# Kernel tuning notes

Hardware: AMD Instinct MI355X
Metric: run time of the kernel (lower is better)

## Reference

```python
import jax, jax.numpy as jnp
import numpy as np

NEG_SLOPE = 0.01  # F.leaky_relu default
EPS = 1e-12       # F.normalize default eps

def _lrelu(h):
    return jnp.where(h > 0, h, NEG_SLOPE * h)

def setup_inputs() -> dict:
    key = jax.random.key(0)
    ks = jax.random.split(key, 16)
    N, E, D = 100000, 800000, 64
    x = jax.random.normal(ks[0], (N, D), dtype=jnp.float32)
    src = jax.random.randint(ks[1], (E,), 0, N, dtype=jnp.int32)
    dst = jax.random.randint(ks[2], (E,), 0, N, dtype=jnp.int32)
    def lin(k, fo, fi):
        k1, k2 = jax.random.split(k)
        s = 1.0 / np.sqrt(fi)
        w = jax.random.uniform(k1, (fo, fi), jnp.float32, -s, s)
        b = jax.random.uniform(k2, (fo,), jnp.float32, -s, s)
        return w, b
    w1, b1 = lin(ks[3], 256, D)
    w2, b2 = lin(ks[4], 128, 256)
    w3, b3 = lin(ks[5], 64, 128)
    w4, b4 = lin(ks[6], 1, 64)
    w_self, _ = lin(ks[7], D, D)   # SAGEConv fc_self (no bias)
    w_neigh, _ = lin(ks[8], D, D)  # SAGEConv fc_neigh (no bias)
    bias = jnp.zeros((D,), jnp.float32)  # SAGEConv bias param
    return dict(x=x, src=src, dst=dst, w1=w1, b1=b1, w2=w2, b2=b2,
                w3=w3, b3=b3, w4=w4, b4=b4,
                w_self=w_self, w_neigh=w_neigh, bias=bias)

def reference(x, src, dst, w1, b1, w2, b2, w3, b3, w4, b4, w_self, w_neigh, bias):
    N = x.shape[0]
    # per-edge score MLP on (h_u - h_v)
    d = x[src] - x[dst]                       # [E, D]
    h = _lrelu(d @ w1.T + b1)                 # [E, 256]
    h = _lrelu(h @ w2.T + b2)                 # [E, 128]
    h = _lrelu(h @ w3.T + b3)                 # [E, 64]
    e = jax.nn.sigmoid(h @ w4.T + b4)         # [E, 1]
    # SAGEConv 'mean' with edge weights: mean over incoming edges of e * x_src
    msg = e * x[src]                          # [E, D]
    s = jax.ops.segment_sum(msg, dst, num_segments=N)               # [N, D]
    deg = jax.ops.segment_sum(jnp.ones((src.shape[0],), x.dtype), dst,
                              num_segments=N)                        # [N]
    neigh = s / jnp.maximum(deg, 1.0)[:, None]
    A = x @ w_self.T + neigh @ w_neigh.T + bias
    A = _lrelu(A)
    norm = jnp.maximum(jnp.linalg.norm(A, axis=1, keepdims=True), EPS)
    A = A / norm
    return A, e
```

## Files before the change

kernel.cpp:

```cpp
#include <hip/hip_runtime.h>
#include <hip/hip_bf16.h>

typedef unsigned short u16;
typedef unsigned int   u32;
typedef __attribute__((ext_vector_type(8))) short short8;
typedef __attribute__((ext_vector_type(4))) float f32x4;

__device__ __forceinline__ u16 f2bf(float f) {
  u32 u = __float_as_uint(f);
  u += 0x7FFFu + ((u >> 16) & 1u);
  return (u16)(u >> 16);
}
__device__ __forceinline__ float bf2f(u16 h) { return __uint_as_float(((u32)h) << 16); }
__device__ __forceinline__ u32 pk2(float lo, float hi) {
  union { __hip_bfloat162 h; u32 u; } c;
  c.h = __float22bfloat162_rn(make_float2(lo, hi));
  return c.u;
}
__device__ __forceinline__ float lo16f(u32 u) { return __uint_as_float(u << 16); }
__device__ __forceinline__ float hi16f(u32 u) { return __uint_as_float(u & 0xffff0000u); }
__device__ __forceinline__ float lrelu(float v) { return v > 0.f ? v : 0.01f * v; }

__host__ __device__ __forceinline__ int sig(int c) {
  return ((c >> 5) << 5) | ((c & 12) << 1) | (((c >> 4) & 1) << 2) | (c & 3);
}

union U8 { u32 w[4]; short8 v; };

#define MFMA16(A, B, C) __builtin_amdgcn_mfma_f32_16x16x32_bf16(A, B, C, 0, 0, 0)

#define W2_BASE 2048
#define W3_BASE 6144
#define NCHUNK8 7168


__global__ __launch_bounds__(512, 2) void edge_mlp(
    const float* __restrict__ x, const int* __restrict__ src, const int* __restrict__ dst,
    const short8* __restrict__ wcat,
    const float* __restrict__ b1p, const float* __restrict__ b2p, const float* __restrict__ b3p,
    const float* __restrict__ w4p, const float* __restrict__ b4,
    const int* __restrict__ rowptr, const int* __restrict__ ord,
    u16* __restrict__ msgbuf, float* __restrict__ eout, int E)
{
  __shared__ short8 ldsw[NCHUNK8];
  const int tid  = threadIdx.x;
  const int lane = tid & 63;
  const int wv   = tid >> 6;
  const int g    = lane >> 4;
  const int r    = lane & 15;
  const int eb   = (blockIdx.x * 8 + wv) * 32;
  const int e0   = eb + r, e1 = eb + 16 + r;
  const int ec0  = e0 < E ? e0 : E - 1;
  const int ec1  = e1 < E ? e1 : E - 1;
  const int sn0 = src[ec0], dn0 = dst[ec0];
  const int sn1 = src[ec1], dn1 = dst[ec1];
  const float b4v = b4[0];

  const float* xsr0 = x + (size_t)sn0 * 64 + 8 * g;
  const float* xdr0 = x + (size_t)dn0 * 64 + 8 * g;
  const float* xsr1 = x + (size_t)sn1 * 64 + 8 * g;
  const float* xdr1 = x + (size_t)dn1 * 64 + 8 * g;
  const float4 a0s0 = *(const float4*)(xsr0),      a0s1 = *(const float4*)(xsr0 + 4);
  const float4 a0s2 = *(const float4*)(xsr0 + 32), a0s3 = *(const float4*)(xsr0 + 36);
  const float4 a0d0 = *(const float4*)(xdr0),      a0d1 = *(const float4*)(xdr0 + 4);
  const float4 a0d2 = *(const float4*)(xdr0 + 32), a0d3 = *(const float4*)(xdr0 + 36);
  const float4 a1s0 = *(const float4*)(xsr1),      a1s1 = *(const float4*)(xsr1 + 4);
  const float4 a1s2 = *(const float4*)(xsr1 + 32), a1s3 = *(const float4*)(xsr1 + 36);
  const float4 a1d0 = *(const float4*)(xdr1),      a1d1 = *(const float4*)(xdr1 + 4);
  const float4 a1d2 = *(const float4*)(xdr1 + 32), a1d3 = *(const float4*)(xdr1 + 36);
  const int pos0 = rowptr[dn0] + ord[ec0];
  const int pos1 = rowptr[dn1] + ord[ec1];

  {
    const short8* gp = wcat + wv * 64 + lane;
    short8*       lp = ldsw + wv * 64;
#pragma unroll
    for (int i = 0; i < 14; i++) {
      __builtin_amdgcn_global_load_lds(
          (const __attribute__((address_space(1))) u32*)(gp + i * 512),
          (__attribute__((address_space(3))) u32*)(lp + i * 512), 16, 0, 0);
    }
  }
  __syncthreads();

  U8 bA0, bB0, bA1, bB1, sA0lo, sA0hi, sA1lo, sA1hi;
  bA0.w[0] = pk2(a0s0.x - a0d0.x, a0s0.y - a0d0.y);
  bA0.w[1] = pk2(a0s0.z - a0d0.z, a0s0.w - a0d0.w);
  bA0.w[2] = pk2(a0s1.x - a0d1.x, a0s1.y - a0d1.y);
  bA0.w[3] = pk2(a0s1.z - a0d1.z, a0s1.w - a0d1.w);
  bB0.w[0] = pk2(a0s2.x - a0d2.x, a0s2.y - a0d2.y);
  bB0.w[1] = pk2(a0s2.z - a0d2.z, a0s2.w - a0d2.w);
  bB0.w[2] = pk2(a0s3.x - a0d3.x, a0s3.y - a0d3.y);
  bB0.w[3] = pk2(a0s3.z - a0d3.z, a0s3.w - a0d3.w);
  bA1.w[0] = pk2(a1s0.x - a1d0.x, a1s0.y - a1d0.y);
  bA1.w[1] = pk2(a1s0.z - a1d0.z, a1s0.w - a1d0.w);
  bA1.w[2] = pk2(a1s1.x - a1d1.x, a1s1.y - a1d1.y);
  bA1.w[3] = pk2(a1s1.z - a1d1.z, a1s1.w - a1d1.w);
  bB1.w[0] = pk2(a1s2.x - a1d2.x, a1s2.y - a1d2.y);
  bB1.w[1] = pk2(a1s2.z - a1d2.z, a1s2.w - a1d2.w);
  bB1.w[2] = pk2(a1s3.x - a1d3.x, a1s3.y - a1d3.y);
  bB1.w[3] = pk2(a1s3.z - a1d3.z, a1s3.w - a1d3.w);
  sA0lo.w[0] = pk2(a0s0.x, a0s0.y); sA0lo.w[1] = pk2(a0s0.z, a0s0.w);
  sA0lo.w[2] = pk2(a0s1.x, a0s1.y); sA0lo.w[3] = pk2(a0s1.z, a0s1.w);
  sA0hi.w[0] = pk2(a0s2.x, a0s2.y); sA0hi.w[1] = pk2(a0s2.z, a0s2.w);
  sA0hi.w[2] = pk2(a0s3.x, a0s3.y); sA0hi.w[3] = pk2(a0s3.z, a0s3.w);
  sA1lo.w[0] = pk2(a1s0.x, a1s0.y); sA1lo.w[1] = pk2(a1s0.z, a1s0.w);
  sA1lo.w[2] = pk2(a1s1.x, a1s1.y); sA1lo.w[3] = pk2(a1s1.z, a1s1.w);
  sA1hi.w[0] = pk2(a1s2.x, a1s2.y); sA1hi.w[1] = pk2(a1s2.z, a1s2.w);
  sA1hi.w[2] = pk2(a1s3.x, a1s3.y); sA1hi.w[3] = pk2(a1s3.z, a1s3.w);

  U8 h1A[8], h1B[8];
  {
    const float* b1l = b1p + 4 * g;
#pragma unroll
    for (int t = 0; t < 16; t++) {
      short8 a0 = ldsw[(t * 2 + 0) * 64 + lane];
      short8 a1 = ldsw[(t * 2 + 1) * 64 + lane];
      f32x4 p = {}, q = {};
      p = MFMA16(a0, bA0.v, p); p = MFMA16(a1, bB0.v, p);
      q = MFMA16(a0, bA1.v, q); q = MFMA16(a1, bB1.v, q);
      float4 bb = *(const float4*)(b1l + 16 * t);
      const int w0 = 2 * t, w1 = 2 * t + 1;
      h1A[w0 >> 2].w[w0 & 3] = pk2(lrelu(p[0] + bb.x), lrelu(p[1] + bb.y));
      h1A[w1 >> 2].w[w1 & 3] = pk2(lrelu(p[2] + bb.z), lrelu(p[3] + bb.w));
      h1B[w0 >> 2].w[w0 & 3] = pk2(lrelu(q[0] + bb.x), lrelu(q[1] + bb.y));
      h1B[w1 >> 2].w[w1 & 3] = pk2(lrelu(q[2] + bb.z), lrelu(q[3] + bb.w));
    }
  }

  U8 h2A[4], h2B[4];
  {
    const float* b2l = b2p + 4 * g;
#pragma unroll
    for (int t = 0; t < 8; t++) {
      f32x4 p = {}, q = {};
#pragma unroll
      for (int s = 0; s < 8; s++) {
        short8 a = ldsw[W2_BASE + (t * 8 + s) * 64 + lane];
        p = MFMA16(a, h1A[s].v, p);
        q = MFMA16(a, h1B[s].v, q);
      }
      float4 bb = *(const float4*)(b2l + 16 * t);
      const int w0 = 2 * t, w1 = 2 * t + 1;
      h2A[w0 >> 2].w[w0 & 3] = pk2(lrelu(p[0] + bb.x), lrelu(p[1] + bb.y));
      h2A[w1 >> 2].w[w1 & 3] = pk2(lrelu(p[2] + bb.z), lrelu(p[3] + bb.w));
      h2B[w0 >> 2].w[w0 & 3] = pk2(lrelu(q[0] + bb.x), lrelu(q[1] + bb.y));
      h2B[w1 >> 2].w[w1 & 3] = pk2(lrelu(q[2] + bb.z), lrelu(q[3] + bb.w));
    }
  }

  float dot0 = 0.f, dot1 = 0.f;
  {
    const float* b3l = b3p + 4 * g;
    const float* w4l = w4p + 4 * g;
#pragma unroll
    for (int t = 0; t < 4; t++) {
      f32x4 p = {}, q = {};
#pragma unroll
      for (int s = 0; s < 4; s++) {
        short8 a = ldsw[W3_BASE + (t * 4 + s) * 64 + lane];
        p = MFMA16(a, h2A[s].v, p);
        q = MFMA16(a, h2B[s].v, q);
      }
      float4 bb = *(const float4*)(b3l + 16 * t);
      float4 ww = *(const float4*)(w4l + 16 * t);
      dot0 += lrelu(p[0] + bb.x) * ww.x + lrelu(p[1] + bb.y) * ww.y
            + lrelu(p[2] + bb.z) * ww.z + lrelu(p[3] + bb.w) * ww.w;
      dot1 += lrelu(q[0] + bb.x) * ww.x + lrelu(q[1] + bb.y) * ww.y
            + lrelu(q[2] + bb.z) * ww.z + lrelu(q[3] + bb.w) * ww.w;
    }
  }
  dot0 += __shfl_xor(dot0, 16); dot0 += __shfl_xor(dot0, 32);
  dot1 += __shfl_xor(dot1, 16); dot1 += __shfl_xor(dot1, 32);
  const float ev0 = 1.f / (1.f + __expf(-(dot0 + b4v)));
  const float ev1 = 1.f / (1.f + __expf(-(dot1 + b4v)));

  if (g == 0) {
    if (e0 < E) eout[e0] = ev0;
    if (e1 < E) eout[e1] = ev1;
  }
  if (e0 < E) {
    u16* mp = msgbuf + (size_t)pos0 * 64 + g * 16;
    U8 m;
    m.w[0] = pk2(ev0 * lo16f(sA0lo.w[0]), ev0 * hi16f(sA0lo.w[0]));
    m.w[1] = pk2(ev0 * lo16f(sA0lo.w[1]), ev0 * hi16f(sA0lo.w[1]));
    m.w[2] = pk2(ev0 * lo16f(sA0lo.w[2]), ev0 * hi16f(sA0lo.w[2]));
    m.w[3] = pk2(ev0 * lo16f(sA0lo.w[3]), ev0 * hi16f(sA0lo.w[3]));
    *(short8*)(mp) = m.v;
    m.w[0] = pk2(ev0 * lo16f(sA0hi.w[0]), ev0 * hi16f(sA0hi.w[0]));
    m.w[1] = pk2(ev0 * lo16f(sA0hi.w[1]), ev0 * hi16f(sA0hi.w[1]));
    m.w[2] = pk2(ev0 * lo16f(sA0hi.w[2]), ev0 * hi16f(sA0hi.w[2]));
    m.w[3] = pk2(ev0 * lo16f(sA0hi.w[3]), ev0 * hi16f(sA0hi.w[3]));
    *(short8*)(mp + 8) = m.v;
  }
  if (e1 < E) {
    u16* mp = msgbuf + (size_t)pos1 * 64 + g * 16;
    U8 m;
    m.w[0] = pk2(ev1 * lo16f(sA1lo.w[0]), ev1 * hi16f(sA1lo.w[0]));
    m.w[1] = pk2(ev1 * lo16f(sA1lo.w[1]), ev1 * hi16f(sA1lo.w[1]));
    m.w[2] = pk2(ev1 * lo16f(sA1lo.w[2]), ev1 * hi16f(sA1lo.w[2]));
    m.w[3] = pk2(ev1 * lo16f(sA1lo.w[3]), ev1 * hi16f(sA1lo.w[3]));
    *(short8*)(mp) = m.v;
    m.w[0] = pk2(ev1 * lo16f(sA1hi.w[0]), ev1 * hi16f(sA1hi.w[0]));
    m.w[1] = pk2(ev1 * lo16f(sA1hi.w[1]), ev1 * hi16f(sA1hi.w[1]));
    m.w[2] = pk2(ev1 * lo16f(sA1hi.w[2]), ev1 * hi16f(sA1hi.w[2]));
    m.w[3] = pk2(ev1 * lo16f(sA1hi.w[3]), ev1 * hi16f(sA1hi.w[3]));
    *(short8*)(mp + 8) = m.v;
  }
}

__global__ void deg_hist(const int* __restrict__ dst, int* __restrict__ degi,
                         int* __restrict__ ord, int E)
{
  const int i = blockIdx.x * 256 + threadIdx.x;
  if (i < E) ord[i] = atomicAdd(&degi[dst[i]], 1);
}

__global__ void scan_part(const int* __restrict__ degi, int* __restrict__ rowptr,
                          int* __restrict__ bsum, int N)
{
  __shared__ int wsum[4];
  const int tid = threadIdx.x, lane = tid & 63, w = tid >> 6;
  const int base = blockIdx.x * 1024 + tid * 4;
  int d0 = 0, d1 = 0, d2 = 0, d3 = 0;
  if (base + 3 < N) {
    int4 v = *(const int4*)(degi + base);
    d0 = v.x; d1 = v.y; d2 = v.z; d3 = v.w;
  } else {
    if (base < N)     d0 = degi[base];
    if (base + 1 < N) d1 = degi[base + 1];
    if (base + 2 < N) d2 = degi[base + 2];
    if (base + 3 < N) d3 = degi[base + 3];
  }
  const int ts = d0 + d1 + d2 + d3;
  int sc = ts;
#pragma unroll
  for (int o = 1; o < 64; o <<= 1) { int v = __shfl_up(sc, o); if (lane >= o) sc += v; }
  if (lane == 63) wsum[w] = sc;
  __syncthreads();
  int woff = 0;
  for (int i = 0; i < w; i++) woff += wsum[i];
  const int ex = woff + sc - ts;
  if (base < N)     rowptr[base]     = ex;
  if (base + 1 < N) rowptr[base + 1] = ex + d0;
  if (base + 2 < N) rowptr[base + 2] = ex + d0 + d1;
  if (base + 3 < N) rowptr[base + 3] = ex + d0 + d1 + d2;
  if (tid == 255) bsum[blockIdx.x] = woff + sc;
}

__global__ void scan_bsum(int* __restrict__ bsum, int nb)
{
  __shared__ int wsum[4];
  const int tid = threadIdx.x, lane = tid & 63, w = tid >> 6;
  const int v = tid < nb ? bsum[tid] : 0;
  int sc = v;
#pragma unroll
  for (int o = 1; o < 64; o <<= 1) { int t = __shfl_up(sc, o); if (lane >= o) sc += t; }
  if (lane == 63) wsum[w] = sc;
  __syncthreads();
  int woff = 0;
  for (int i = 0; i < w; i++) woff += wsum[i];
  if (tid < nb) bsum[tid] = woff + sc - v;
}

__global__ void scan_add(int* __restrict__ rowptr, const int* __restrict__ bsum,
                         int N, int E)
{
  const int base = blockIdx.x * 1024 + threadIdx.x * 4;
  const int off = bsum[blockIdx.x];
#pragma unroll
  for (int i = 0; i < 4; i++)
    if (base + i < N) rowptr[base + i] += off;
  if (blockIdx.x == 0 && threadIdx.x == 0) rowptr[N] = E;
}

__global__ __launch_bounds__(256, 4) void node_agg_mfma(
    const float* __restrict__ x, const u16* __restrict__ msgbuf,
    const int* __restrict__ rowptr, const short8* __restrict__ wfin,
    const float* __restrict__ bias, float* __restrict__ A, int N)
{
  __shared__ short8 ldsW[1024];
  __shared__ float  nbuf[4][16][68];
  const int tid = threadIdx.x, wv = tid >> 6, lane = tid & 63;
  const int g = lane >> 4, r = lane & 15;
  for (int i = tid; i < 1024; i += 256) ldsW[i] = wfin[i];

  const int n0 = (blockIdx.x * 4 + wv) * 16;
  const int nr = (n0 + r) < N ? (n0 + r) : N - 1;
  const float* xp = x + (size_t)nr * 64 + 8 * g;
  const float4 xf0 = *(const float4*)(xp);
  const float4 xf1 = *(const float4*)(xp + 4);
  const float4 xf2 = *(const float4*)(xp + 32);
  const float4 xf3 = *(const float4*)(xp + 36);
  int rp = 0;
  if (lane < 17) rp = rowptr[min(n0 + lane, N)];
  const int cch = (((lane >> 3) & 1) << 5) | ((lane >> 4) << 3) | (lane & 7);
  for (int rr = 0; rr < 16; rr++) {
    const int s = __shfl(rp, rr);
    const int t = __shfl(rp, rr + 1);
    float acc = 0.f;
    for (int j = s; j < t; j += 4) {
      const int j1 = (j + 1 < t) ? j + 1 : j;
      const int j2 = (j + 2 < t) ? j + 2 : j;
      const int j3 = (j + 3 < t) ? j + 3 : j;
      const float v0 = bf2f(msgbuf[(size_t)j  * 64 + lane]);
      const float v1 = bf2f(msgbuf[(size_t)j1 * 64 + lane]);
      const float v2 = bf2f(msgbuf[(size_t)j2 * 64 + lane]);
      const float v3 = bf2f(msgbuf[(size_t)j3 * 64 + lane]);
      const float m1 = (j + 1 < t) ? 1.f : 0.f;
      const float m2 = (j + 2 < t) ? 1.f : 0.f;
      const float m3 = (j + 3 < t) ? 1.f : 0.f;
      acc += v0 + m1 * v1 + m2 * v2 + m3 * v3;
    }
    const float inv = 1.f / fmaxf((float)(t - s), 1.f);
    nbuf[wv][rr][cch] = acc * inv;
  }
  __syncthreads();

  U8 bf0, bf1, bf2q, bf3q;
  bf0.w[0] = pk2(xf0.x, xf0.y); bf0.w[1] = pk2(xf0.z, xf0.w);
  bf0.w[2] = pk2(xf1.x, xf1.y); bf0.w[3] = pk2(xf1.z, xf1.w);
  bf1.w[0] = pk2(xf2.x, xf2.y); bf1.w[1] = pk2(xf2.z, xf2.w);
  bf1.w[2] = pk2(xf3.x, xf3.y); bf1.w[3] = pk2(xf3.z, xf3.w);
  {
    const float* nb = nbuf[wv][r];
    const float4 n0v = *(const float4*)(nb + 8 * g);
    const float4 n1v = *(const float4*)(nb + 8 * g + 4);
    const float4 n2v = *(const float4*)(nb + 32 + 8 * g);
    const float4 n3v = *(const float4*)(nb + 32 + 8 * g + 4);
    bf2q.w[0] = pk2(n0v.x, n0v.y); bf2q.w[1] = pk2(n0v.z, n0v.w);
    bf2q.w[2] = pk2(n1v.x, n1v.y); bf2q.w[3] = pk2(n1v.z, n1v.w);
    bf3q.w[0] = pk2(n2v.x, n2v.y); bf3q.w[1] = pk2(n2v.z, n2v.w);
    bf3q.w[2] = pk2(n3v.x, n3v.y); bf3q.w[3] = pk2(n3v.z, n3v.w);
  }

  f32x4 acct[4] = {};
#pragma unroll
  for (int t = 0; t < 4; t++) {
    acct[t] = MFMA16(ldsW[(t * 4 + 0) * 64 + lane], bf0.v,  acct[t]);
    acct[t] = MFMA16(ldsW[(t * 4 + 1) * 64 + lane], bf1.v,  acct[t]);
    acct[t] = MFMA16(ldsW[(t * 4 + 2) * 64 + lane], bf2q.v, acct[t]);
    acct[t] = MFMA16(ldsW[(t * 4 + 3) * 64 + lane], bf3q.v, acct[t]);
  }

  f32x4 av[4];
  float ss = 0.f;
#pragma unroll
  for (int t = 0; t < 4; t++) {
    const float4 bb = *(const float4*)(bias + 16 * t + 4 * g);
    av[t][0] = lrelu(acct[t][0] + bb.x);
    av[t][1] = lrelu(acct[t][1] + bb.y);
    av[t][2] = lrelu(acct[t][2] + bb.z);
    av[t][3] = lrelu(acct[t][3] + bb.w);
    ss += av[t][0] * av[t][0] + av[t][1] * av[t][1]
        + av[t][2] * av[t][2] + av[t][3] * av[t][3];
  }
  ss += __shfl_xor(ss, 16); ss += __shfl_xor(ss, 32);
  const float rn = 1.f / fmaxf(sqrtf(ss), 1e-12f);
  if (n0 + r < N) {
    float* ap = A + (size_t)(n0 + r) * 64 + 4 * g;
#pragma unroll
    for (int t = 0; t < 4; t++) {
      float4 o;
      o.x = av[t][0] * rn; o.y = av[t][1] * rn;
      o.z = av[t][2] * rn; o.w = av[t][3] * rn;
      *(float4*)(ap + 16 * t) = o;
    }
  }
}

__global__ void convert_w(const float* __restrict__ w1, const float* __restrict__ w2,
                          const float* __restrict__ w3,
                          const float* __restrict__ b1, const float* __restrict__ b2,
                          const float* __restrict__ b3, const float* __restrict__ w4,
                          const float* __restrict__ w_self, const float* __restrict__ w_neigh,
                          u16* __restrict__ wcat, u16* __restrict__ wfin,
                          float* __restrict__ b1p, float* __restrict__ b2p,
                          float* __restrict__ b3p, float* __restrict__ w4p)
{
  const int idx = blockIdx.x * 256 + threadIdx.x;
  if (idx < 57344) {
    const float* w; int K, nsteps, loc;
    if (idx < 16384)      { loc = idx;         w = w1; K = 64;  nsteps = 2; }
    else if (idx < 49152) { loc = idx - 16384; w = w2; K = 256; nsteps = 8; }
    else                  { loc = idx - 49152; w = w3; K = 128; nsteps = 4; }
    const int chunk = loc >> 9;
    const int lane  = (loc >> 3) & 63;
    const int j     = loc & 7;
    const int t = chunk / nsteps, s = chunk % nsteps;
    const int m = sig(t * 16 + (lane & 15));
    const int k = s * 32 + (lane >> 4) * 8 + j;
    wcat[idx] = f2bf(w[m * K + k]);
  } else if (idx < 65536) {
    const int o = idx - 57344;
    const int c = o >> 9, lane = (o >> 3) & 63, j = o & 7;
    const int t = c >> 2, s = c & 3;
    const int m = 16 * t + (lane & 15);
    const int k = 32 * s + ((lane >> 4) << 3) + j;
    wfin[o] = f2bf(k < 64 ? w_self[m * 64 + k] : w_neigh[m * 64 + (k - 64)]);
  }
  if (idx < 256) b1p[idx] = b1[sig(idx)];
  if (idx < 128) b2p[idx] = b2[sig(idx)];
  if (idx < 64)  { b3p[idx] = b3[sig(idx)]; w4p[idx] = w4[sig(idx)]; }
}

extern "C" void kernel_launch(void* const* d_in, const int* in_sizes, int n_in,
                              void* d_out, int out_size, void* d_ws, size_t ws_size,
                              hipStream_t stream)
{
  const float* x       = (const float*)d_in[0];
  const int*   src     = (const int*)d_in[1];
  const int*   dst     = (const int*)d_in[2];
  const float* w1      = (const float*)d_in[3];
  const float* b1      = (const float*)d_in[4];
  const float* w2      = (const float*)d_in[5];
  const float* b2      = (const float*)d_in[6];
  const float* w3      = (const float*)d_in[7];
  const float* b3      = (const float*)d_in[8];
  const float* w4      = (const float*)d_in[9];
  const float* b4      = (const float*)d_in[10];
  const float* w_self  = (const float*)d_in[11];
  const float* w_neigh = (const float*)d_in[12];
  const float* bias    = (const float*)d_in[13];

  const int N = in_sizes[0] / 64;
  const int E = in_sizes[1];

  float* A    = (float*)d_out;
  float* eout = (float*)d_out + (size_t)N * 64;

  char* ws = (char*)d_ws;
  size_t off = 0;
  auto alloc = [&](size_t bytes) {
    void* p = ws + off;
    off = (off + bytes + 255) & ~(size_t)255;
    return p;
  };
  int*    degi   = (int*)alloc((size_t)N * 4);
  int*    rowptr = (int*)alloc((size_t)(N + 1) * 4);
  int*    ord    = (int*)alloc((size_t)E * 4);
  int*    bsum   = (int*)alloc(1024 * 4);
  short8* wcat   = (short8*)alloc((size_t)57344 * 2);
  short8* wfin   = (short8*)alloc((size_t)8192 * 2);
  float*  b1p    = (float*)alloc(256 * 4);
  float*  b2p    = (float*)alloc(128 * 4);
  float*  b3p    = (float*)alloc(64 * 4);
  float*  w4p    = (float*)alloc(64 * 4);
  u16*    msgbuf = (u16*)alloc((size_t)E * 128);

  hipMemsetAsync(degi, 0, (size_t)N * sizeof(int), stream);

  convert_w<<<256, 256, 0, stream>>>(w1, w2, w3, b1, b2, b3, w4, w_self, w_neigh,
                                     (u16*)wcat, (u16*)wfin, b1p, b2p, b3p, w4p);

  deg_hist<<<(E + 255) / 256, 256, 0, stream>>>(dst, degi, ord, E);

  const int nsb = (N + 1023) / 1024;
  scan_part<<<nsb, 256, 0, stream>>>(degi, rowptr, bsum, N);
  scan_bsum<<<1, 256, 0, stream>>>(bsum, nsb);
  scan_add<<<nsb, 256, 0, stream>>>(rowptr, bsum, N, E);

  const int nblk = (E + 255) / 256;
  edge_mlp<<<nblk, 512, 0, stream>>>(x, src, dst, wcat, b1p, b2p, b3p, w4p, b4,
                                     rowptr, ord, msgbuf, eout, E);

  const int nblk2 = (N + 63) / 64;
  node_agg_mfma<<<nblk2, 256, 0, stream>>>(x, msgbuf, rowptr, wfin, bias, A, N);
}
```

Measured before the change: 296.7 us.

## Stream MLP weights from global/L2 into registers instead of staging in LDS

```diff
diff --git a/kernel.cpp b/kernel.cpp
--- a/kernel.cpp
+++ b/kernel.cpp
@@ -31,10 +31,9 @@
 
 #define W2_BASE 2048
 #define W3_BASE 6144
-#define NCHUNK8 7168
-
-
-__global__ __launch_bounds__(512, 2) void edge_mlp(
+
+
+__global__ __launch_bounds__(256, 4) void edge_mlp(
     const float* __restrict__ x, const int* __restrict__ src, const int* __restrict__ dst,
     const short8* __restrict__ wcat,
     const float* __restrict__ b1p, const float* __restrict__ b2p, const float* __restrict__ b3p,
@@ -42,13 +41,12 @@
     const int* __restrict__ rowptr, const int* __restrict__ ord,
     u16* __restrict__ msgbuf, float* __restrict__ eout, int E)
 {
-  __shared__ short8 ldsw[NCHUNK8];
   const int tid  = threadIdx.x;
   const int lane = tid & 63;
   const int wv   = tid >> 6;
   const int g    = lane >> 4;
   const int r    = lane & 15;
-  const int eb   = (blockIdx.x * 8 + wv) * 32;
+  const int eb   = (blockIdx.x * 4 + wv) * 32;
   const int e0   = eb + r, e1 = eb + 16 + r;
   const int ec0  = e0 < E ? e0 : E - 1;
   const int ec1  = e1 < E ? e1 : E - 1;
@@ -71,17 +69,8 @@
   const int pos0 = rowptr[dn0] + ord[ec0];
   const int pos1 = rowptr[dn1] + ord[ec1];
 
-  {
-    const short8* gp = wcat + wv * 64 + lane;
-    short8*       lp = ldsw + wv * 64;
-#pragma unroll
-    for (int i = 0; i < 14; i++) {
-      __builtin_amdgcn_global_load_lds(
-          (const __attribute__((address_space(1))) u32*)(gp + i * 512),
-          (__attribute__((address_space(3))) u32*)(lp + i * 512), 16, 0, 0);
-    }
-  }
-  __syncthreads();
+  short8 w1f0 = wcat[lane];
+  short8 w1f1 = wcat[64 + lane];
 
   U8 bA0, bB0, bA1, bB1, sA0lo, sA0hi, sA1lo, sA1hi;
   bA0.w[0] = pk2(a0s0.x - a0d0.x, a0s0.y - a0d0.y);
@@ -114,8 +103,11 @@
     const float* b1l = b1p + 4 * g;
 #pragma unroll
     for (int t = 0; t < 16; t++) {
-      short8 a0 = ldsw[(t * 2 + 0) * 64 + lane];
-      short8 a1 = ldsw[(t * 2 + 1) * 64 + lane];
+      short8 a0 = w1f0, a1 = w1f1;
+      if (t < 15) {
+        w1f0 = wcat[(2 * t + 2) * 64 + lane];
+        w1f1 = wcat[(2 * t + 3) * 64 + lane];
+      }
       f32x4 p = {}, q = {};
       p = MFMA16(a0, bA0.v, p); p = MFMA16(a1, bB0.v, p);
       q = MFMA16(a0, bA1.v, q); q = MFMA16(a1, bB1.v, q);
@@ -130,13 +122,17 @@
 
   U8 h2A[4], h2B[4];
   {
+    short8 w2f[8];
+#pragma unroll
+    for (int s = 0; s < 8; s++) w2f[s] = wcat[W2_BASE + s * 64 + lane];
     const float* b2l = b2p + 4 * g;
 #pragma unroll
     for (int t = 0; t < 8; t++) {
       f32x4 p = {}, q = {};
 #pragma unroll
       for (int s = 0; s < 8; s++) {
-        short8 a = ldsw[W2_BASE + (t * 8 + s) * 64 + lane];
+        short8 a = w2f[s];
+        if (t < 7) w2f[s] = wcat[W2_BASE + ((t + 1) * 8 + s) * 64 + lane];
         p = MFMA16(a, h1A[s].v, p);
         q = MFMA16(a, h1B[s].v, q);
       }
@@ -151,6 +147,9 @@
 
   float dot0 = 0.f, dot1 = 0.f;
   {
+    short8 w3f[4];
+#pragma unroll
+    for (int s = 0; s < 4; s++) w3f[s] = wcat[W3_BASE + s * 64 + lane];
     const float* b3l = b3p + 4 * g;
     const float* w4l = w4p + 4 * g;
 #pragma unroll
@@ -158,7 +157,8 @@
       f32x4 p = {}, q = {};
 #pragma unroll
       for (int s = 0; s < 4; s++) {
-        short8 a = ldsw[W3_BASE + (t * 4 + s) * 64 + lane];
+        short8 a = w3f[s];
+        if (t < 3) w3f[s] = wcat[W3_BASE + ((t + 1) * 4 + s) * 64 + lane];
         p = MFMA16(a, h2A[s].v, p);
         q = MFMA16(a, h2B[s].v, q);
       }
@@ -460,8 +460,8 @@
   scan_bsum<<<1, 256, 0, stream>>>(bsum, nsb);
   scan_add<<<nsb, 256, 0, stream>>>(rowptr, bsum, N, E);
 
-  const int nblk = (E + 255) / 256;
-  edge_mlp<<<nblk, 512, 0, stream>>>(x, src, dst, wcat, b1p, b2p, b3p, w4p, b4,
+  const int nblk = (E + 127) / 128;
+  edge_mlp<<<nblk, 256, 0, stream>>>(x, src, dst, wcat, b1p, b2p, b3p, w4p, b4,
                                      rowptr, ord, msgbuf, eout, E);
 
   const int nblk2 = (N + 63) / 64;
```

Result: slower. 869.9 us (+193.2%).

## Process 64 edges per wave in edge MLP to amortize weight LDS reads

Applied to the files above, without the earlier changes.

```diff
diff --git a/kernel.cpp b/kernel.cpp
--- a/kernel.cpp
+++ b/kernel.cpp
@@ -17,8 +17,6 @@
   c.h = __float22bfloat162_rn(make_float2(lo, hi));
   return c.u;
 }
-__device__ __forceinline__ float lo16f(u32 u) { return __uint_as_float(u << 16); }
-__device__ __forceinline__ float hi16f(u32 u) { return __uint_as_float(u & 0xffff0000u); }
 __device__ __forceinline__ float lrelu(float v) { return v > 0.f ? v : 0.01f * v; }
 
 __host__ __device__ __forceinline__ int sig(int c) {
@@ -34,7 +32,7 @@
 #define NCHUNK8 7168
 
 
-__global__ __launch_bounds__(512, 2) void edge_mlp(
+__global__ __launch_bounds__(512, 1) void edge_mlp(
     const float* __restrict__ x, const int* __restrict__ src, const int* __restrict__ dst,
     const short8* __restrict__ wcat,
     const float* __restrict__ b1p, const float* __restrict__ b2p, const float* __restrict__ b3p,
@@ -48,28 +46,30 @@
   const int wv   = tid >> 6;
   const int g    = lane >> 4;
   const int r    = lane & 15;
-  const int eb   = (blockIdx.x * 8 + wv) * 32;
-  const int e0   = eb + r, e1 = eb + 16 + r;
-  const int ec0  = e0 < E ? e0 : E - 1;
-  const int ec1  = e1 < E ? e1 : E - 1;
-  const int sn0 = src[ec0], dn0 = dst[ec0];
-  const int sn1 = src[ec1], dn1 = dst[ec1];
+  const int eb   = (blockIdx.x * 8 + wv) * 64;
   const float b4v = b4[0];
 
-  const float* xsr0 = x + (size_t)sn0 * 64 + 8 * g;
-  const float* xdr0 = x + (size_t)dn0 * 64 + 8 * g;
-  const float* xsr1 = x + (size_t)sn1 * 64 + 8 * g;
-  const float* xdr1 = x + (size_t)dn1 * 64 + 8 * g;
-  const float4 a0s0 = *(const float4*)(xsr0),      a0s1 = *(const float4*)(xsr0 + 4);
-  const float4 a0s2 = *(const float4*)(xsr0 + 32), a0s3 = *(const float4*)(xsr0 + 36);
-  const float4 a0d0 = *(const float4*)(xdr0),      a0d1 = *(const float4*)(xdr0 + 4);
-  const float4 a0d2 = *(const float4*)(xdr0 + 32), a0d3 = *(const float4*)(xdr0 + 36);
-  const float4 a1s0 = *(const float4*)(xsr1),      a1s1 = *(const float4*)(xsr1 + 4);
-  const float4 a1s2 = *(const float4*)(xsr1 + 32), a1s3 = *(const float4*)(xsr1 + 36);
-  const float4 a1d0 = *(const float4*)(xdr1),      a1d1 = *(const float4*)(xdr1 + 4);
-  const float4 a1d2 = *(const float4*)(xdr1 + 32), a1d3 = *(const float4*)(xdr1 + 36);
-  const int pos0 = rowptr[dn0] + ord[ec0];
-  const int pos1 = rowptr[dn1] + ord[ec1];
+  int e[4], ec[4], sn[4], dn[4], pos[4];
+#pragma unroll
+  for (int c = 0; c < 4; c++) {
+    e[c]  = eb + 16 * c + r;
+    ec[c] = e[c] < E ? e[c] : E - 1;
+    sn[c] = src[ec[c]];
+    dn[c] = dst[ec[c]];
+  }
+
+  float4 xs[4][4], xd[4][4];
+#pragma unroll
+  for (int c = 0; c < 4; c++) {
+    const float* xsr = x + (size_t)sn[c] * 64 + 8 * g;
+    const float* xdr = x + (size_t)dn[c] * 64 + 8 * g;
+    xs[c][0] = *(const float4*)(xsr);      xs[c][1] = *(const float4*)(xsr + 4);
+    xs[c][2] = *(const float4*)(xsr + 32); xs[c][3] = *(const float4*)(xsr + 36);
+    xd[c][0] = *(const float4*)(xdr);      xd[c][1] = *(const float4*)(xdr + 4);
+    xd[c][2] = *(const float4*)(xdr + 32); xd[c][3] = *(const float4*)(xdr + 36);
+  }
+#pragma unroll
+  for (int c = 0; c < 4; c++) pos[c] = rowptr[dn[c]] + ord[ec[c]];
 
   {
     const short8* gp = wcat + wv * 64 + lane;
@@ -83,129 +83,128 @@
   }
   __syncthreads();
 
-  U8 bA0, bB0, bA1, bB1, sA0lo, sA0hi, sA1lo, sA1hi;
-  bA0.w[0] = pk2(a0s0.x - a0d0.x, a0s0.y - a0d0.y);
-  bA0.w[1] = pk2(a0s0.z - a0d0.z, a0s0.w - a0d0.w);
-  bA0.w[2] = pk2(a0s1.x - a0d1.x, a0s1.y - a0d1.y);
-  bA0.w[3] = pk2(a0s1.z - a0d1.z, a0s1.w - a0d1.w);
-  bB0.w[0] = pk2(a0s2.x - a0d2.x, a0s2.y - a0d2.y);
-  bB0.w[1] = pk2(a0s2.z - a0d2.z, a0s2.w - a0d2.w);
-  bB0.w[2] = pk2(a0s3.x - a0d3.x, a0s3.y - a0d3.y);
-  bB0.w[3] = pk2(a0s3.z - a0d3.z, a0s3.w - a0d3.w);
-  bA1.w[0] = pk2(a1s0.x - a1d0.x, a1s0.y - a1d0.y);
-  bA1.w[1] = pk2(a1s0.z - a1d0.z, a1s0.w - a1d0.w);
-  bA1.w[2] = pk2(a1s1.x - a1d1.x, a1s1.y - a1d1.y);
-  bA1.w[3] = pk2(a1s1.z - a1d1.z, a1s1.w - a1d1.w);
-  bB1.w[0] = pk2(a1s2.x - a1d2.x, a1s2.y - a1d2.y);
-  bB1.w[1] = pk2(a1s2.z - a1d2.z, a1s2.w - a1d2.w);
-  bB1.w[2] = pk2(a1s3.x - a1d3.x, a1s3.y - a1d3.y);
-  bB1.w[3] = pk2(a1s3.z - a1d3.z, a1s3.w - a1d3.w);
-  sA0lo.w[0] = pk2(a0s0.x, a0s0.y); sA0lo.w[1] = pk2(a0s0.z, a0s0.w);
-  sA0lo.w[2] = pk2(a0s1.x, a0s1.y); sA0lo.w[3] = pk2(a0s1.z, a0s1.w);
-  sA0hi.w[0] = pk2(a0s2.x, a0s2.y); sA0hi.w[1] = pk2(a0s2.z, a0s2.w);
-  sA0hi.w[2] = pk2(a0s3.x, a0s3.y); sA0hi.w[3] = pk2(a0s3.z, a0s3.w);
-  sA1lo.w[0] = pk2(a1s0.x, a1s0.y); sA1lo.w[1] = pk2(a1s0.z, a1s0.w);
-  sA1lo.w[2] = pk2(a1s1.x, a1s1.y); sA1lo.w[3] = pk2(a1s1.z, a1s1.w);
-  sA1hi.w[0] = pk2(a1s2.x, a1s2.y); sA1hi.w[1] = pk2(a1s2.z, a1s2.w);
-  sA1hi.w[2] = pk2(a1s3.x, a1s3.y); sA1hi.w[3] = pk2(a1s3.z, a1s3.w);
-
-  U8 h1A[8], h1B[8];
+  U8 bA[4], bB[4];
+#pragma unroll
+  for (int c = 0; c < 4; c++) {
+    bA[c].w[0] = pk2(xs[c][0].x - xd[c][0].x, xs[c][0].y - xd[c][0].y);
+    bA[c].w[1] = pk2(xs[c][0].z - xd[c][0].z, xs[c][0].w - xd[c][0].w);
+    bA[c].w[2] = pk2(xs[c][1].x - xd[c][1].x, xs[c][1].y - xd[c][1].y);
+    bA[c].w[3] = pk2(xs[c][1].z - xd[c][1].z, xs[c][1].w - xd[c][1].w);
+    bB[c].w[0] = pk2(xs[c][2].x - xd[c][2].x, xs[c][2].y - xd[c][2].y);
+    bB[c].w[1] = pk2(xs[c][2].z - xd[c][2].z, xs[c][2].w - xd[c][2].w);
+    bB[c].w[2] = pk2(xs[c][3].x - xd[c][3].x, xs[c][3].y - xd[c][3].y);
+    bB[c].w[3] = pk2(xs[c][3].z - xd[c][3].z, xs[c][3].w - xd[c][3].w);
+  }
+
+  U8 h1[4][8];
   {
     const float* b1l = b1p + 4 * g;
 #pragma unroll
     for (int t = 0; t < 16; t++) {
       short8 a0 = ldsw[(t * 2 + 0) * 64 + lane];
       short8 a1 = ldsw[(t * 2 + 1) * 64 + lane];
-      f32x4 p = {}, q = {};
-      p = MFMA16(a0, bA0.v, p); p = MFMA16(a1, bB0.v, p);
-      q = MFMA16(a0, bA1.v, q); q = MFMA16(a1, bB1.v, q);
       float4 bb = *(const float4*)(b1l + 16 * t);
       const int w0 = 2 * t, w1 = 2 * t + 1;
-      h1A[w0 >> 2].w[w0 & 3] = pk2(lrelu(p[0] + bb.x), lrelu(p[1] + bb.y));
-      h1A[w1 >> 2].w[w1 & 3] = pk2(lrelu(p[2] + bb.z), lrelu(p[3] + bb.w));
-      h1B[w0 >> 2].w[w0 & 3] = pk2(lrelu(q[0] + bb.x), lrelu(q[1] + bb.y));
-      h1B[w1 >> 2].w[w1 & 3] = pk2(lrelu(q[2] + bb.z), lrelu(q[3] + bb.w));
-    }
-  }
-
-  U8 h2A[4], h2B[4];
+#pragma unroll
+      for (int c = 0; c < 4; c++) {
+        f32x4 p = {};
+        p = MFMA16(a0, bA[c].v, p);
+        p = MFMA16(a1, bB[c].v, p);
+        h1[c][w0 >> 2].w[w0 & 3] = pk2(lrelu(p[0] + bb.x), lrelu(p[1] + bb.y));
+        h1[c][w1 >> 2].w[w1 & 3] = pk2(lrelu(p[2] + bb.z), lrelu(p[3] + bb.w));
+      }
+    }
+  }
+
+  U8 h2[4][4];
   {
     const float* b2l = b2p + 4 * g;
 #pragma unroll
     for (int t = 0; t < 8; t++) {
-      f32x4 p = {}, q = {};
+      f32x4 p0 = {}, p1 = {}, p2 = {}, p3 = {};
 #pragma unroll
       for (int s = 0; s < 8; s++) {
         short8 a = ldsw[W2_BASE + (t * 8 + s) * 64 + lane];
-        p = MFMA16(a, h1A[s].v, p);
-        q = MFMA16(a, h1B[s].v, q);
+        p0 = MFMA16(a, h1[0][s].v, p0);
+        p1 = MFMA16(a, h1[1][s].v, p1);
+        p2 = MFMA16(a, h1[2][s].v, p2);
+        p3 = MFMA16(a, h1[3][s].v, p3);
       }
       float4 bb = *(const float4*)(b2l + 16 * t);
       const int w0 = 2 * t, w1 = 2 * t + 1;
-      h2A[w0 >> 2].w[w0 & 3] = pk2(lrelu(p[0] + bb.x), lrelu(p[1] + bb.y));
-      h2A[w1 >> 2].w[w1 & 3] = pk2(lrelu(p[2] + bb.z), lrelu(p[3] + bb.w));
-      h2B[w0 >> 2].w[w0 & 3] = pk2(lrelu(q[0] + bb.x), lrelu(q[1] + bb.y));
-      h2B[w1 >> 2].w[w1 & 3] = pk2(lrelu(q[2] + bb.z), lrelu(q[3] + bb.w));
-    }
-  }
-
-  float dot0 = 0.f, dot1 = 0.f;
+      h2[0][w0 >> 2].w[w0 & 3] = pk2(lrelu(p0[0] + bb.x), lrelu(p0[1] + bb.y));
+      h2[0][w1 >> 2].w[w1 & 3] = pk2(lrelu(p0[2] + bb.z), lrelu(p0[3] + bb.w));
+      h2[1][w0 >> 2].w[w0 & 3] = pk2(lrelu(p1[0] + bb.x), lrelu(p1[1] + bb.y));
+      h2[1][w1 >> 2].w[w1 & 3] = pk2(lrelu(p1[2] + bb.z), lrelu(p1[3] + bb.w));
+      h2[2][w0 >> 2].w[w0 & 3] = pk2(lrelu(p2[0] + bb.x), lrelu(p2[1] + bb.y));
+      h2[2][w1 >> 2].w[w1 & 3] = pk2(lrelu(p2[2] + bb.z), lrelu(p2[3] + bb.w));
+      h2[3][w0 >> 2].w[w0 & 3] = pk2(lrelu(p3[0] + bb.x), lrelu(p3[1] + bb.y));
+      h2[3][w1 >> 2].w[w1 & 3] = pk2(lrelu(p3[2] + bb.z), lrelu(p3[3] + bb.w));
+    }
+  }
+
+  float dot[4] = {0.f, 0.f, 0.f, 0.f};
   {
     const float* b3l = b3p + 4 * g;
     const float* w4l = w4p + 4 * g;
 #pragma unroll
     for (int t = 0; t < 4; t++) {
-      f32x4 p = {}, q = {};
+      f32x4 p0 = {}, p1 = {}, p2 = {}, p3 = {};
 #pragma unroll
       for (int s = 0; s < 4; s++) {
         short8 a = ldsw[W3_BASE + (t * 4 + s) * 64 + lane];
-        p = MFMA16(a, h2A[s].v, p);
-        q = MFMA16(a, h2B[s].v, q);
+        p0 = MFMA16(a, h2[0][s].v, p0);
+        p1 = MFMA16(a, h2[1][s].v, p1);
+        p2 = MFMA16(a, h2[2][s].v, p2);
+        p3 = MFMA16(a, h2[3][s].v, p3);
       }
       float4 bb = *(const float4*)(b3l + 16 * t);
       float4 ww = *(const float4*)(w4l + 16 * t);
-      dot0 += lrelu(p[0] + bb.x) * ww.x + lrelu(p[1] + bb.y) * ww.y
-            + lrelu(p[2] + bb.z) * ww.z + lrelu(p[3] + bb.w) * ww.w;
-      dot1 += lrelu(q[0] + bb.x) * ww.x + lrelu(q[1] + bb.y) * ww.y
-            + lrelu(q[2] + bb.z) * ww.z + lrelu(q[3] + bb.w) * ww.w;
-    }
-  }
-  dot0 += __shfl_xor(dot0, 16); dot0 += __shfl_xor(dot0, 32);
-  dot1 += __shfl_xor(dot1, 16); dot1 += __shfl_xor(dot1, 32);
-  const float ev0 = 1.f / (1.f + __expf(-(dot0 + b4v)));
-  const float ev1 = 1.f / (1.f + __expf(-(dot1 + b4v)));
+      dot[0] += lrelu(p0[0] + bb.x) * ww.x + lrelu(p0[1] + bb.y) * ww.y
+              + lrelu(p0[2] + bb.z) * ww.z + lrelu(p0[3] + bb.w) * ww.w;
+      dot[1] += lrelu(p1[0] + bb.x) * ww.x + lrelu(p1[1] + bb.y) * ww.y
+              + lrelu(p1[2] + bb.z) * ww.z + lrelu(p1[3] + bb.w) * ww.w;
+      dot[2] += lrelu(p2[0] + bb.x) * ww.x + lrelu(p2[1] + bb.y) * ww.y
+              + lrelu(p2[2] + bb.z) * ww.z + lrelu(p2[3] + bb.w) * ww.w;
+      dot[3] += lrelu(p3[0] + bb.x) * ww.x + lrelu(p3[1] + bb.y) * ww.y
+              + lrelu(p3[2] + bb.z) * ww.z + lrelu(p3[3] + bb.w) * ww.w;
+    }
+  }
+  float ev[4];
+#pragma unroll
+  for (int c = 0; c < 4; c++) {
+    float d = dot[c];
+    d += __shfl_xor(d, 16);
+    d += __shfl_xor(d, 32);
+    ev[c] = 1.f / (1.f + __expf(-(d + b4v)));
+  }
 
   if (g == 0) {
-    if (e0 < E) eout[e0] = ev0;
-    if (e1 < E) eout[e1] = ev1;
-  }
-  if (e0 < E) {
-    u16* mp = msgbuf + (size_t)pos0 * 64 + g * 16;
-    U8 m;
-    m.w[0] = pk2(ev0 * lo16f(sA0lo.w[0]), ev0 * hi16f(sA0lo.w[0]));
-    m.w[1] = pk2(ev0 * lo16f(sA0lo.w[1]), ev0 * hi16f(sA0lo.w[1]));
-    m.w[2] = pk2(ev0 * lo16f(sA0lo.w[2]), ev0 * hi16f(sA0lo.w[2]));
-    m.w[3] = pk2(ev0 * lo16f(sA0lo.w[3]), ev0 * hi16f(sA0lo.w[3]));
-    *(short8*)(mp) = m.v;
-    m.w[0] = pk2(ev0 * lo16f(sA0hi.w[0]), ev0 * hi16f(sA0hi.w[0]));
-    m.w[1] = pk2(ev0 * lo16f(sA0hi.w[1]), ev0 * hi16f(sA0hi.w[1]));
-    m.w[2] = pk2(ev0 * lo16f(sA0hi.w[2]), ev0 * hi16f(sA0hi.w[2]));
-    m.w[3] = pk2(ev0 * lo16f(sA0hi.w[3]), ev0 * hi16f(sA0hi.w[3]));
-    *(short8*)(mp + 8) = m.v;
-  }
-  if (e1 < E) {
-    u16* mp = msgbuf + (size_t)pos1 * 64 + g * 16;
-    U8 m;
-    m.w[0] = pk2(ev1 * lo16f(sA1lo.w[0]), ev1 * hi16f(sA1lo.w[0]));
-    m.w[1] = pk2(ev1 * lo16f(sA1lo.w[1]), ev1 * hi16f(sA1lo.w[1]));
-    m.w[2] = pk2(ev1 * lo16f(sA1lo.w[2]), ev1 * hi16f(sA1lo.w[2]));
-    m.w[3] = pk2(ev1 * lo16f(sA1lo.w[3]), ev1 * hi16f(sA1lo.w[3]));
-    *(short8*)(mp) = m.v;
-    m.w[0] = pk2(ev1 * lo16f(sA1hi.w[0]), ev1 * hi16f(sA1hi.w[0]));
-    m.w[1] = pk2(ev1 * lo16f(sA1hi.w[1]), ev1 * hi16f(sA1hi.w[1]));
-    m.w[2] = pk2(ev1 * lo16f(sA1hi.w[2]), ev1 * hi16f(sA1hi.w[2]));
-    m.w[3] = pk2(ev1 * lo16f(sA1hi.w[3]), ev1 * hi16f(sA1hi.w[3]));
-    *(short8*)(mp + 8) = m.v;
+#pragma unroll
+    for (int c = 0; c < 4; c++)
+      if (e[c] < E) eout[e[c]] = ev[c];
+  }
+#pragma unroll
+  for (int c = 0; c < 4; c++) {
+    if (e[c] < E) {
+      const float* xsr = x + (size_t)sn[c] * 64 + 8 * g;
+      const float4 v0 = *(const float4*)(xsr);
+      const float4 v1 = *(const float4*)(xsr + 4);
+      const float4 v2 = *(const float4*)(xsr + 32);
+      const float4 v3 = *(const float4*)(xsr + 36);
+      u16* mp = msgbuf + (size_t)pos[c] * 64 + g * 16;
+      U8 m;
+      m.w[0] = pk2(ev[c] * v0.x, ev[c] * v0.y);
+      m.w[1] = pk2(ev[c] * v0.z, ev[c] * v0.w);
+      m.w[2] = pk2(ev[c] * v1.x, ev[c] * v1.y);
+      m.w[3] = pk2(ev[c] * v1.z, ev[c] * v1.w);
+      *(short8*)(mp) = m.v;
+      m.w[0] = pk2(ev[c] * v2.x, ev[c] * v2.y);
+      m.w[1] = pk2(ev[c] * v2.z, ev[c] * v2.w);
+      m.w[2] = pk2(ev[c] * v3.x, ev[c] * v3.y);
+      m.w[3] = pk2(ev[c] * v3.z, ev[c] * v3.w);
+      *(short8*)(mp + 8) = m.v;
+    }
   }
 }
 
@@ -460,7 +459,7 @@
   scan_bsum<<<1, 256, 0, stream>>>(bsum, nsb);
   scan_add<<<nsb, 256, 0, stream>>>(rowptr, bsum, N, E);
 
-  const int nblk = (E + 255) / 256;
+  const int nblk = (E + 511) / 512;
   edge_mlp<<<nblk, 512, 0, stream>>>(x, src, dst, wcat, b1p, b2p, b3p, w4p, b4,
                                      rowptr, ord, msgbuf, eout, E);
 
```

After: 305.3 us. 1.03x slower.
